# Performance work log

Measured on AMD Instinct MI355X. Metric: run time of the kernel, lower is better.

Reference implementation:

```python
import jax, jax.numpy as jnp
import numpy as np

N = 50000      # nodes
E = 800000     # directed edges (before self-loops)
IN = 128       # input feature dim
HID = 32       # per-head hidden channels
HEADS = 4
OUT = 16       # output classes
NEG_SLOPE = 0.2


def setup_inputs() -> dict:
    key = jax.random.key(0)
    ks = jax.random.split(key, 14)
    x = jax.random.normal(ks[0], (N, IN), jnp.float32)
    edge_index = jax.random.randint(ks[1], (2, E), 0, N, dtype=jnp.int64)

    def glorot(k, shape):
        fan = shape[0] + shape[-1]
        s = np.sqrt(6.0 / fan).astype(np.float32)
        return jax.random.uniform(k, shape, jnp.float32, -s, s)

    return {
        "x": x,
        "edge_index": edge_index,
        # layer 0: IN -> HEADS*HID
        "W1": glorot(ks[2], (IN, HEADS * HID)),
        "a_src1": glorot(ks[3], (HEADS, HID)),
        "a_dst1": glorot(ks[4], (HEADS, HID)),
        "b1": jnp.zeros((HEADS * HID,), jnp.float32),
        # layer 1: HEADS*HID -> HEADS*HID
        "W2": glorot(ks[5], (HEADS * HID, HEADS * HID)),
        "a_src2": glorot(ks[6], (HEADS, HID)),
        "a_dst2": glorot(ks[7], (HEADS, HID)),
        "b2": jnp.zeros((HEADS * HID,), jnp.float32),
        # layer 2: HEADS*HID -> OUT, heads=1
        "W3": glorot(ks[8], (HEADS * HID, OUT)),
        "a_src3": glorot(ks[9], (1, OUT)),
        "a_dst3": glorot(ks[10], (1, OUT)),
        "b3": jnp.zeros((OUT,), jnp.float32),
    }


def _gat_layer(x, src, dst, W, a_s, a_d, b):
    """One PyG-style GATConv (eval mode). src/dst include self-loops."""
    H, C = a_s.shape
    h = (x @ W).reshape(N, H, C)                       # [N,H,C]
    e_src = jnp.einsum('nhc,hc->nh', h, a_s)           # [N,H]
    e_dst = jnp.einsum('nhc,hc->nh', h, a_d)
    e = jax.nn.leaky_relu(e_src[src] + e_dst[dst], NEG_SLOPE)   # [E',H]
    # segment softmax over incoming edges of each target node
    m = jax.ops.segment_max(e, dst, num_segments=N)    # [N,H]
    p = jnp.exp(e - m[dst])
    denom = jax.ops.segment_sum(p, dst, num_segments=N)
    alpha = p / (denom[dst] + 1e-16)                   # [E',H]
    out = jax.ops.segment_sum(alpha[:, :, None] * h[src], dst, num_segments=N)
    return out.reshape(N, H * C) + b


def reference(x, edge_index, W1, a_src1, a_dst1, b1, W2, a_src2, a_dst2, b2,
              W3, a_src3, a_dst3, b3):
    loops = jnp.arange(N, dtype=edge_index.dtype)
    src = jnp.concatenate([edge_index[0], loops])
    dst = jnp.concatenate([edge_index[1], loops])
    h = jax.nn.relu(_gat_layer(x, src, dst, W1, a_src1, a_dst1, b1))
    h = jax.nn.relu(_gat_layer(h, src, dst, W2, a_src2, a_dst2, b2))
    return _gat_layer(h, src, dst, W3, a_src3, a_dst3, b3)   # [N, OUT]
```

## Files before the change

### kernel.cpp

```cpp
#include <hip/hip_runtime.h>

#define NODES 50000
#define EDGES 800000
#define EPLUS (EDGES + NODES)
#define GEMMBLK 782
#define FILLBLK 3321
#define CAP 64

__device__ __forceinline__ float ld_f(const void* p, int isbf, size_t i) {
    if (isbf) return __uint_as_float(((unsigned)((const unsigned short*)p)[i]) << 16);
    return ((const float*)p)[i];
}
__device__ __forceinline__ int ld_idx(const int* ei, int i64, int elem) {
    int v = i64 ? ei[(size_t)elem * 2] : ei[elem];
    v = v < 0 ? 0 : v;
    return v >= NODES ? NODES - 1 : v;
}
__device__ __forceinline__ unsigned short f2bf(float f) {
    unsigned u = __float_as_uint(f);
    u = u + 0x7FFFu + ((u >> 16) & 1u);
    return (unsigned short)(u >> 16);
}
__device__ __forceinline__ unsigned pack2bf(float a, float b) {
    return (unsigned)f2bf(a) | ((unsigned)f2bf(b) << 16);
}
__device__ __forceinline__ float bflo(unsigned u) { return __uint_as_float(u << 16); }
__device__ __forceinline__ float bfhi(unsigned u) { return __uint_as_float(u & 0xFFFF0000u); }

__device__ __forceinline__ void detect_flags(const unsigned* xw, const int* eiw,
                                             int* sh, int& isbf, int& i64) {
    const int t = threadIdx.x;
    if (t < 2) sh[t] = 0;
    __syncthreads();
    if (t < 256) {
        unsigned lo = xw[t] & 0xFFFFu;
        int e = (int)((lo >> 7) & 0xFF);
        if (lo == 0u || (e >= 90 && e <= 140)) atomicAdd(&sh[0], 1);
    }
    if (t < 64) {
        if (eiw[2 * t + 1] == 0) atomicAdd(&sh[1], 1);
    }
    __syncthreads();
    isbf = sh[0] > 200 ? 1 : 0;
    i64  = sh[1] > 48 ? 1 : 0;
}

#define O_W1 0
#define O_AS1 16384
#define O_AD1 16512
#define O_B1 16640
#define O_W2 16768
#define O_AS2 33152
#define O_AD2 33280
#define O_B2 33408
#define O_W3 33536
#define O_AS3 35584
#define O_AD3 35600
#define O_B3 35616
#define W_TOTAL 35632

__global__ __launch_bounds__(256, 4) void k_fillgemm1(
        const unsigned* __restrict__ xraw, const int* __restrict__ ei,
        const void* w1, const void* as1, const void* ad1, const void* b1,
        const void* w2, const void* as2, const void* ad2, const void* b2,
        const void* w3, const void* as3, const void* ad3, const void* b3,
        float* __restrict__ Wc,
        unsigned short* __restrict__ hout, float* __restrict__ es, float* __restrict__ ed,
        int* __restrict__ cnt, unsigned short* __restrict__ col) {
    __shared__ int sh[2];
    const int t = threadIdx.x;
    int isbf, i64;
    detect_flags(xraw, ei, sh, isbf, i64);

    if (blockIdx.x >= GEMMBLK) {
        const int f = (blockIdx.x - GEMMBLK) * 256 + t;
        if (f < W_TOTAL) {
            const int sz[12] = {16384,128,128,128,16384,128,128,128,2048,16,16,16};
            const void* ps[12] = {w1,as1,ad1,b1,w2,as2,ad2,b2,w3,as3,ad3,b3};
            int off = 0;
#pragma unroll
            for (int s = 0; s < 12; ++s) {
                if (f >= off && f < off + sz[s]) Wc[f] = ld_f(ps[s], isbf, f - off);
                off += sz[s];
            }
        }
        if (f >= EPLUS) return;
        int s, d;
        if (f < EDGES) {
            s = ld_idx(ei, i64, f);
            d = ld_idx(ei, i64, EDGES + f);
        } else s = d = f - EDGES;
        int slot = atomicAdd(&cnt[d], 1);
        if (slot < CAP) col[d * CAP + slot] = (unsigned short)s;
        return;
    }

    __shared__ float Xl[32][68];
    __shared__ float Wl[32][128];
    const int rowBase = blockIdx.x * 64;
    const int tx = t & 15, ty = t >> 4;
    const int cA = tx * 4, cB = 64 + tx * 4;

    float acc[4][8];
#pragma unroll
    for (int r = 0; r < 4; ++r)
#pragma unroll
        for (int j = 0; j < 8; ++j) acc[r][j] = 0.f;

    for (int k0 = 0; k0 < 128; k0 += 32) {
        __syncthreads();
        if (!isbf) {
            const float4* Wg = (const float4*)((const float*)w1 + k0 * 128);
            float4* Wl4 = (float4*)&Wl[0][0];
#pragma unroll
            for (int j = 0; j < 4; ++j) Wl4[t + 256 * j] = Wg[t + 256 * j];
#pragma unroll
            for (int j = 0; j < 2; ++j) {
                int f = t + 256 * j;
                int r = f >> 3;
                int kk = (f & 7) * 4;
                int gr = rowBase + r;
                if (gr >= NODES) gr = NODES - 1;
                float4 v = *(const float4*)((const float*)xraw + (size_t)gr * 128 + k0 + kk);
                Xl[kk][r] = v.x; Xl[kk+1][r] = v.y; Xl[kk+2][r] = v.z; Xl[kk+3][r] = v.w;
            }
        } else {
            float* Wf = &Wl[0][0];
#pragma unroll
            for (int j = 0; j < 4; ++j) {
                int f = t + 256 * j;
#pragma unroll
                for (int i = 0; i < 4; ++i)
                    Wf[f * 4 + i] = ld_f(w1, 1, (size_t)(k0 * 128) + f * 4 + i);
            }
#pragma unroll
            for (int j = 0; j < 2; ++j) {
                int f = t + 256 * j;
                int r = f >> 3;
                int kk = (f & 7) * 4;
                int gr = rowBase + r;
                if (gr >= NODES) gr = NODES - 1;
#pragma unroll
                for (int i = 0; i < 4; ++i)
                    Xl[kk + i][r] = ld_f(xraw, 1, (size_t)gr * 128 + k0 + kk + i);
            }
        }
        __syncthreads();
#pragma unroll 4
        for (int k = 0; k < 32; ++k) {
            const float4 xa = *(const float4*)&Xl[k][ty * 4];
            const float4 wa = *(const float4*)&Wl[k][cA];
            const float4 wb = *(const float4*)&Wl[k][cB];
            const float xs[4] = {xa.x, xa.y, xa.z, xa.w};
            const float ws[8] = {wa.x, wa.y, wa.z, wa.w, wb.x, wb.y, wb.z, wb.w};
#pragma unroll
            for (int r = 0; r < 4; ++r)
#pragma unroll
                for (int j = 0; j < 8; ++j)
                    acc[r][j] += xs[r] * ws[j];
        }
    }

    float asA[4], asB[4], adA[4], adB[4];
#pragma unroll
    for (int j = 0; j < 4; ++j) {
        asA[j] = ld_f(as1, isbf, cA + j); asB[j] = ld_f(as1, isbf, cB + j);
        adA[j] = ld_f(ad1, isbf, cA + j); adB[j] = ld_f(ad1, isbf, cB + j);
    }
    const int hA = tx >> 3;
#pragma unroll
    for (int r = 0; r < 4; ++r) {
        const int row = rowBase + ty * 4 + r;
        const bool ok = row < NODES;
        if (ok) {
            uint2 pA = {pack2bf(acc[r][0], acc[r][1]), pack2bf(acc[r][2], acc[r][3])};
            uint2 pB = {pack2bf(acc[r][4], acc[r][5]), pack2bf(acc[r][6], acc[r][7])};
            *(uint2*)&hout[(size_t)row * 128 + cA] = pA;
            *(uint2*)&hout[(size_t)row * 128 + cB] = pB;
        }
        float seA = acc[r][0]*asA[0] + acc[r][1]*asA[1] + acc[r][2]*asA[2] + acc[r][3]*asA[3];
        float seB = acc[r][4]*asB[0] + acc[r][5]*asB[1] + acc[r][6]*asB[2] + acc[r][7]*asB[3];
        float sdA = acc[r][0]*adA[0] + acc[r][1]*adA[1] + acc[r][2]*adA[2] + acc[r][3]*adA[3];
        float sdB = acc[r][4]*adB[0] + acc[r][5]*adB[1] + acc[r][6]*adB[2] + acc[r][7]*adB[3];
#pragma unroll
        for (int off = 1; off < 8; off <<= 1) {
            seA += __shfl_xor(seA, off);
            seB += __shfl_xor(seB, off);
            sdA += __shfl_xor(sdA, off);
            sdB += __shfl_xor(sdB, off);
        }
        if (ok && (tx & 7) == 0) {
            es[row * 4 + hA]     = seA;
            es[row * 4 + 2 + hA] = seB;
            ed[row * 4 + hA]     = sdA;
            ed[row * 4 + 2 + hA] = sdB;
        }
    }
}

__global__ __launch_bounds__(256, 4) void k_gemm128(
        const unsigned short* __restrict__ in, const float* __restrict__ W,
        const float* __restrict__ a_s, const float* __restrict__ a_d,
        unsigned short* __restrict__ hout, float* __restrict__ es, float* __restrict__ ed) {
    __shared__ float Xl[32][68];
    __shared__ float Wl[32][128];
    const int t = threadIdx.x;
    const int rowBase = blockIdx.x * 64;
    const int tx = t & 15, ty = t >> 4;
    const int cA = tx * 4, cB = 64 + tx * 4;

    float acc[4][8];
#pragma unroll
    for (int r = 0; r < 4; ++r)
#pragma unroll
        for (int j = 0; j < 8; ++j) acc[r][j] = 0.f;

    for (int k0 = 0; k0 < 128; k0 += 32) {
        __syncthreads();
        const float4* Wg = (const float4*)(W + k0 * 128);
        float4* Wl4 = (float4*)&Wl[0][0];
#pragma unroll
        for (int j = 0; j < 4; ++j) Wl4[t + 256 * j] = Wg[t + 256 * j];
#pragma unroll
        for (int j = 0; j < 2; ++j) {
            int f = t + 256 * j;
            int r = f >> 3;
            int kk = (f & 7) * 4;
            int gr = rowBase + r;
            if (gr >= NODES) gr = NODES - 1;
            uint2 v = *(const uint2*)(in + (size_t)gr * 128 + k0 + kk);
            Xl[kk][r] = bflo(v.x); Xl[kk+1][r] = bfhi(v.x);
            Xl[kk+2][r] = bflo(v.y); Xl[kk+3][r] = bfhi(v.y);
        }
        __syncthreads();
#pragma unroll 4
        for (int k = 0; k < 32; ++k) {
            const float4 xa = *(const float4*)&Xl[k][ty * 4];
            const float4 wa = *(const float4*)&Wl[k][cA];
            const float4 wb = *(const float4*)&Wl[k][cB];
            const float xs[4] = {xa.x, xa.y, xa.z, xa.w};
            const float ws[8] = {wa.x, wa.y, wa.z, wa.w, wb.x, wb.y, wb.z, wb.w};
#pragma unroll
            for (int r = 0; r < 4; ++r)
#pragma unroll
                for (int j = 0; j < 8; ++j)
                    acc[r][j] += xs[r] * ws[j];
        }
    }

    float asA[4], asB[4], adA[4], adB[4];
#pragma unroll
    for (int j = 0; j < 4; ++j) {
        asA[j] = a_s[cA + j]; asB[j] = a_s[cB + j];
        adA[j] = a_d[cA + j]; adB[j] = a_d[cB + j];
    }
    const int hA = tx >> 3;
#pragma unroll
    for (int r = 0; r < 4; ++r) {
        const int row = rowBase + ty * 4 + r;
        const bool ok = row < NODES;
        if (ok) {
            uint2 pA = {pack2bf(acc[r][0], acc[r][1]), pack2bf(acc[r][2], acc[r][3])};
            uint2 pB = {pack2bf(acc[r][4], acc[r][5]), pack2bf(acc[r][6], acc[r][7])};
            *(uint2*)&hout[(size_t)row * 128 + cA] = pA;
            *(uint2*)&hout[(size_t)row * 128 + cB] = pB;
        }
        float seA = acc[r][0]*asA[0] + acc[r][1]*asA[1] + acc[r][2]*asA[2] + acc[r][3]*asA[3];
        float seB = acc[r][4]*asB[0] + acc[r][5]*asB[1] + acc[r][6]*asB[2] + acc[r][7]*asB[3];
        float sdA = acc[r][0]*adA[0] + acc[r][1]*adA[1] + acc[r][2]*adA[2] + acc[r][3]*adA[3];
        float sdB = acc[r][4]*adB[0] + acc[r][5]*adB[1] + acc[r][6]*adB[2] + acc[r][7]*adB[3];
#pragma unroll
        for (int off = 1; off < 8; off <<= 1) {
            seA += __shfl_xor(seA, off);
            seB += __shfl_xor(seB, off);
            sdA += __shfl_xor(sdA, off);
            sdB += __shfl_xor(sdB, off);
        }
        if (ok && (tx & 7) == 0) {
            es[row * 4 + hA]     = seA;
            es[row * 4 + 2 + hA] = seB;
            ed[row * 4 + hA]     = sdA;
            ed[row * 4 + 2 + hA] = sdB;
        }
    }
}

__global__ __launch_bounds__(256, 2) void k_gemm16(
        const unsigned short* __restrict__ in, const float* __restrict__ W,
        const float* __restrict__ a_s, const float* __restrict__ a_d,
        unsigned short* __restrict__ hout, float* __restrict__ es, float* __restrict__ ed) {
    __shared__ float Xl[32][132];
    __shared__ float Wl[128 * 16];
    const int t = threadIdx.x;
    const int rowBase = blockIdx.x * 128;
    const int tx = t & 3, ty = t >> 2;

    ((float4*)Wl)[t] = ((const float4*)W)[t];
    ((float4*)Wl)[t + 256] = ((const float4*)W)[t + 256];

    float acc[2][4];
#pragma unroll
    for (int r = 0; r < 2; ++r)
#pragma unroll
        for (int j = 0; j < 4; ++j) acc[r][j] = 0.f;

    for (int k0 = 0; k0 < 128; k0 += 32) {
        __syncthreads();
#pragma unroll
        for (int j = 0; j < 4; ++j) {
            int f = t + 256 * j;
            int r = f >> 3;
            int kk = (f & 7) * 4;
            int gr = rowBase + r;
            if (gr >= NODES) gr = NODES - 1;
            uint2 v = *(const uint2*)(in + (size_t)gr * 128 + k0 + kk);
            Xl[kk][r] = bflo(v.x); Xl[kk+1][r] = bfhi(v.x);
            Xl[kk+2][r] = bflo(v.y); Xl[kk+3][r] = bfhi(v.y);
        }
        __syncthreads();
#pragma unroll 4
        for (int k = 0; k < 32; ++k) {
            const float2 xv = *(const float2*)&Xl[k][ty * 2];
            const float4 wv = *(const float4*)&Wl[(k0 + k) * 16 + tx * 4];
            acc[0][0] += xv.x * wv.x; acc[0][1] += xv.x * wv.y;
            acc[0][2] += xv.x * wv.z; acc[0][3] += xv.x * wv.w;
            acc[1][0] += xv.y * wv.x; acc[1][1] += xv.y * wv.y;
            acc[1][2] += xv.y * wv.z; acc[1][3] += xv.y * wv.w;
        }
    }

    const float4 asv = *(const float4*)&a_s[tx * 4];
    const float4 adv = *(const float4*)&a_d[tx * 4];
#pragma unroll
    for (int r = 0; r < 2; ++r) {
        const int row = rowBase + ty * 2 + r;
        const bool ok = row < NODES;
        if (ok) {
            uint2 pk = {pack2bf(acc[r][0], acc[r][1]), pack2bf(acc[r][2], acc[r][3])};
            *(uint2*)&hout[(size_t)row * 16 + tx * 4] = pk;
        }
        float se = acc[r][0]*asv.x + acc[r][1]*asv.y + acc[r][2]*asv.z + acc[r][3]*asv.w;
        float sd = acc[r][0]*adv.x + acc[r][1]*adv.y + acc[r][2]*adv.z + acc[r][3]*adv.w;
#pragma unroll
        for (int off = 1; off < 4; off <<= 1) {
            se += __shfl_xor(se, off);
            sd += __shfl_xor(sd, off);
        }
        if (ok && tx == 0) { es[row] = se; ed[row] = sd; }
    }
}

__global__ void k_gather4(const int* __restrict__ cnt, const unsigned short* __restrict__ col,
                          const float* __restrict__ es, const float* __restrict__ ed,
                          const unsigned short* __restrict__ hfeat,
                          const float* __restrict__ bias, unsigned short* __restrict__ outb) {
    const int nd = blockIdx.x * 4 + (threadIdx.x >> 6);
    if (nd >= NODES) return;
    const int lane = threadIdx.x & 63;
    int deg = cnt[nd]; deg = deg < CAP ? deg : CAP;
    const int start = nd * CAP;

    const int esub = lane >> 4;
    const int c = lane & 15;
    const int myh = c >> 2;
    const float edh = ed[nd * 4 + myh];
    const uint4* __restrict__ h4 = (const uint4*)hfeat;
    float a[8] = {0.f,0.f,0.f,0.f,0.f,0.f,0.f,0.f};
    float den = 0.f;

    int e = esub;
    for (; e + 4 < deg; e += 8) {
        int s0 = col[start + e];
        int s1 = col[start + e + 4];
        uint4 u0 = h4[(size_t)s0 * 16 + c];
        uint4 u1 = h4[(size_t)s1 * 16 + c];
        float v0 = es[s0 * 4 + myh] + edh; v0 = v0 > 0.f ? v0 : 0.2f * v0;
        float v1 = es[s1 * 4 + myh] + edh; v1 = v1 > 0.f ? v1 : 0.2f * v1;
        float p0 = __expf(v0);
        float p1 = __expf(v1);
        den += p0 + p1;
        a[0] += p0 * bflo(u0.x) + p1 * bflo(u1.x);
        a[1] += p0 * bfhi(u0.x) + p1 * bfhi(u1.x);
        a[2] += p0 * bflo(u0.y) + p1 * bflo(u1.y);
        a[3] += p0 * bfhi(u0.y) + p1 * bfhi(u1.y);
        a[4] += p0 * bflo(u0.z) + p1 * bflo(u1.z);
        a[5] += p0 * bfhi(u0.z) + p1 * bfhi(u1.z);
        a[6] += p0 * bflo(u0.w) + p1 * bflo(u1.w);
        a[7] += p0 * bfhi(u0.w) + p1 * bfhi(u1.w);
    }
    for (; e < deg; e += 4) {
        int s0 = col[start + e];
        uint4 u0 = h4[(size_t)s0 * 16 + c];
        float v0 = es[s0 * 4 + myh] + edh; v0 = v0 > 0.f ? v0 : 0.2f * v0;
        float p0 = __expf(v0);
        den += p0;
        a[0] += p0 * bflo(u0.x);
        a[1] += p0 * bfhi(u0.x);
        a[2] += p0 * bflo(u0.y);
        a[3] += p0 * bfhi(u0.y);
        a[4] += p0 * bflo(u0.z);
        a[5] += p0 * bfhi(u0.z);
        a[6] += p0 * bflo(u0.w);
        a[7] += p0 * bfhi(u0.w);
    }
    den += __shfl_xor(den, 16);
    den += __shfl_xor(den, 32);
#pragma unroll
    for (int j = 0; j < 8; ++j) {
        a[j] += __shfl_xor(a[j], 16);
        a[j] += __shfl_xor(a[j], 32);
    }

    if (esub == 0) {
        const float inv = 1.f / (den + 1e-16f);
        float4 b0 = ((const float4*)bias)[c * 2];
        float4 b1 = ((const float4*)bias)[c * 2 + 1];
        float o0 = a[0]*inv + b0.x, o1 = a[1]*inv + b0.y;
        float o2 = a[2]*inv + b0.z, o3 = a[3]*inv + b0.w;
        float o4 = a[4]*inv + b1.x, o5 = a[5]*inv + b1.y;
        float o6 = a[6]*inv + b1.z, o7 = a[7]*inv + b1.w;
        o0 = o0 > 0.f ? o0 : 0.f;  o1 = o1 > 0.f ? o1 : 0.f;
        o2 = o2 > 0.f ? o2 : 0.f;  o3 = o3 > 0.f ? o3 : 0.f;
        o4 = o4 > 0.f ? o4 : 0.f;  o5 = o5 > 0.f ? o5 : 0.f;
        o6 = o6 > 0.f ? o6 : 0.f;  o7 = o7 > 0.f ? o7 : 0.f;
        uint4 pk = {pack2bf(o0, o1), pack2bf(o2, o3), pack2bf(o4, o5), pack2bf(o6, o7)};
        ((uint4*)outb)[(size_t)nd * 16 + c] = pk;
    }
}

__global__ void k_gather1(const int* __restrict__ cnt, const unsigned short* __restrict__ col,
                          const float* __restrict__ es, const float* __restrict__ ed,
                          const unsigned short* __restrict__ hfeat,
                          const float* __restrict__ bias, float* __restrict__ outf) {
    const int nd = blockIdx.x * 4 + (threadIdx.x >> 6);
    if (nd >= NODES) return;
    const int lane = threadIdx.x & 63;
    int deg = cnt[nd]; deg = deg < CAP ? deg : CAP;
    const int start = nd * CAP;

    const float edv = ed[nd];
    const int esub = lane >> 3;
    const int c = lane & 7;
    const unsigned* __restrict__ h1 = (const unsigned*)hfeat;
    float a0 = 0.f, a1 = 0.f, den = 0.f;

    int e = esub;
    for (; e + 8 < deg; e += 16) {
        int s0 = col[start + e];
        int s1 = col[start + e + 8];
        unsigned u0 = h1[(size_t)s0 * 8 + c];
        unsigned u1 = h1[(size_t)s1 * 8 + c];
        float v0 = es[s0] + edv; v0 = v0 > 0.f ? v0 : 0.2f * v0;
        float v1 = es[s1] + edv; v1 = v1 > 0.f ? v1 : 0.2f * v1;
        float p0 = __expf(v0);
        float p1 = __expf(v1);
        den += p0 + p1;
        a0 += p0 * bflo(u0) + p1 * bflo(u1);
        a1 += p0 * bfhi(u0) + p1 * bfhi(u1);
    }
    for (; e < deg; e += 8) {
        int s0 = col[start + e];
        unsigned u0 = h1[(size_t)s0 * 8 + c];
        float v0 = es[s0] + edv; v0 = v0 > 0.f ? v0 : 0.2f * v0;
        float p0 = __expf(v0);
        den += p0;
        a0 += p0 * bflo(u0);
        a1 += p0 * bfhi(u0);
    }
    den += __shfl_xor(den, 8);  a0 += __shfl_xor(a0, 8);  a1 += __shfl_xor(a1, 8);
    den += __shfl_xor(den, 16); a0 += __shfl_xor(a0, 16); a1 += __shfl_xor(a1, 16);
    den += __shfl_xor(den, 32); a0 += __shfl_xor(a0, 32); a1 += __shfl_xor(a1, 32);
    if (lane < 8) {
        const float inv = 1.f / (den + 1e-16f);
        float2 b = ((const float2*)bias)[c];
        ((float2*)outf)[(size_t)nd * 8 + c] = make_float2(a0 * inv + b.x, a1 * inv + b.y);
    }
}

static inline int gs(long n) { return (int)((n + 255) / 256); }

extern "C" void kernel_launch(void* const* d_in, const int* in_sizes, int n_in,
                              void* d_out, int out_size, void* d_ws, size_t ws_size,
                              hipStream_t stream) {
    const int* ei = (const int*)d_in[1];
    const unsigned* xraw = (const unsigned*)d_in[0];
    float* out = (float*)d_out;

    char* p = (char*)d_ws;
    unsigned short* Xb  = (unsigned short*)p; p += (size_t)NODES * 128 * 2;
    unsigned short* A   = (unsigned short*)p; p += (size_t)NODES * 128 * 2;
    float*          es  = (float*)p;          p += (size_t)NODES * 4 * 4;
    float*          ed  = (float*)p;          p += (size_t)NODES * 4 * 4;
    float*          Wc  = (float*)p;          p += (size_t)W_TOTAL * 4;
    int*            cnt = (int*)p;            p += (size_t)NODES * 4;
    unsigned short* col = (unsigned short*)p; p += (size_t)NODES * CAP * 2;

    hipMemsetAsync(cnt, 0, (size_t)NODES * 4, stream);

    k_fillgemm1<<<GEMMBLK + FILLBLK, 256, 0, stream>>>(
        xraw, ei,
        d_in[2], d_in[3], d_in[4], d_in[5],
        d_in[6], d_in[7], d_in[8], d_in[9],
        d_in[10], d_in[11], d_in[12], d_in[13],
        Wc, A, es, ed, cnt, col);

    const int ggrid = (NODES + 3) / 4;
    k_gather4<<<ggrid, 256, 0, stream>>>(cnt, col, es, ed, A, Wc + O_B1, Xb);
    k_gemm128<<<(NODES + 63) / 64, 256, 0, stream>>>(Xb, Wc + O_W2, Wc + O_AS2, Wc + O_AD2,
                                                     A, es, ed);
    k_gather4<<<ggrid, 256, 0, stream>>>(cnt, col, es, ed, A, Wc + O_B2, Xb);
    k_gemm16<<<(NODES + 127) / 128, 256, 0, stream>>>(Xb, Wc + O_W3, Wc + O_AS3, Wc + O_AD3,
                                                      A, es, ed);
    k_gather1<<<ggrid, 256, 0, stream>>>(cnt, col, es, ed, A, Wc + O_B3, out);
}
```

Before: 286.4 us.

## Move the three dense GEMMs onto bf16 MFMA with split hi/lo weights

The scalar FP32 tiled GEMMs for all three layers become MFMA 16x16x32 bf16 kernels. A new prep kernel converts the weights into fragment-ordered hi/lo bf16 pairs, and for fp32 inputs the first layer's activations are split the same way, so an error-compensated three-product scheme keeps accuracy close to fp32. The prep kernel also takes over zeroing the edge counters and the weight copy, which removes the separate memset. This adds an extra launch and extra MFMA work for the compensation terms, and activation stores become scalar 16-bit writes instead of packed ones.

```diff
diff --git a/kernel.cpp b/kernel.cpp
--- a/kernel.cpp
+++ b/kernel.cpp
@@ -6,6 +6,10 @@
 #define GEMMBLK 782
 #define FILLBLK 3321
 #define CAP 64
+
+typedef __attribute__((ext_vector_type(8))) short bf16x8;
+typedef __attribute__((ext_vector_type(4))) float f32x4;
+typedef __attribute__((ext_vector_type(4))) short short4v;
 
 __device__ __forceinline__ float ld_f(const void* p, int isbf, size_t i) {
     if (isbf) return __uint_as_float(((unsigned)((const unsigned short*)p)[i]) << 16);
@@ -59,12 +63,71 @@
 #define O_B3 35616
 #define W_TOTAL 35632
 
-__global__ __launch_bounds__(256, 4) void k_fillgemm1(
+#define PB_CNT 196
+#define PB_WC 140
+#define PB_F1 64
+#define PB_F2 64
+#define PB_F3 8
+#define PREP_GRID (PB_CNT + PB_WC + PB_F1 + PB_F2 + PB_F3)
+
+__global__ __launch_bounds__(256) void k_prep(
         const unsigned* __restrict__ xraw, const int* __restrict__ ei,
         const void* w1, const void* as1, const void* ad1, const void* b1,
         const void* w2, const void* as2, const void* ad2, const void* b2,
         const void* w3, const void* as3, const void* ad3, const void* b3,
-        float* __restrict__ Wc,
+        float* __restrict__ Wc, int* __restrict__ cnt,
+        unsigned short* __restrict__ W1fh, unsigned short* __restrict__ W1fl,
+        unsigned short* __restrict__ W2fh, unsigned short* __restrict__ W2fl,
+        unsigned short* __restrict__ W3fh, unsigned short* __restrict__ W3fl) {
+    __shared__ int sh[2];
+    const int t = threadIdx.x;
+    int isbf, i64;
+    detect_flags(xraw, ei, sh, isbf, i64);
+    (void)i64;
+
+    int b = blockIdx.x;
+    if (b < PB_CNT) {
+        int i = b * 256 + t;
+        if (i < NODES) cnt[i] = 0;
+        return;
+    }
+    b -= PB_CNT;
+    if (b < PB_WC) {
+        const int f = b * 256 + t;
+        if (f < W_TOTAL) {
+            const int sz[12] = {16384,128,128,128,16384,128,128,128,2048,16,16,16};
+            const void* ps[12] = {w1,as1,ad1,b1,w2,as2,ad2,b2,w3,as3,ad3,b3};
+            int off = 0;
+#pragma unroll
+            for (int s = 0; s < 12; ++s) {
+                if (f >= off && f < off + sz[s]) Wc[f] = ld_f(ps[s], isbf, f - off);
+                off += sz[s];
+            }
+        }
+        return;
+    }
+    b -= PB_WC;
+    const void* wsrc; unsigned short *fh, *fl; int ncols; int e;
+    if (b < PB_F1)                { wsrc = w1; fh = W1fh; fl = W1fl; ncols = 128; e = b * 256 + t; }
+    else if (b < PB_F1 + PB_F2)   { wsrc = w2; fh = W2fh; fl = W2fl; ncols = 128; e = (b - PB_F1) * 256 + t; }
+    else                          { wsrc = w3; fh = W3fh; fl = W3fl; ncols = 16;  e = (b - PB_F1 - PB_F2) * 256 + t; }
+    const int j = e & 7, l = (e >> 3) & 63;
+    int nf, kc;
+    if (ncols == 128) { nf = (e >> 9) & 7; kc = e >> 12; }
+    else              { nf = 0;            kc = (e >> 9) & 3; }
+    const int k = kc * 32 + (l >> 4) * 4 + (j & 3) + (j >> 2) * 16;
+    const int n = nf * 16 + (l & 15);
+    const float v = ld_f(wsrc, isbf, (size_t)k * ncols + n);
+    const unsigned short hi = f2bf(v);
+    const float res = v - __uint_as_float(((unsigned)hi) << 16);
+    fh[e] = hi;
+    fl[e] = f2bf(res);
+}
+
+__global__ __launch_bounds__(256, 4) void k_fillgemm1(
+        const unsigned* __restrict__ xraw, const int* __restrict__ ei,
+        const unsigned short* __restrict__ W1fh, const unsigned short* __restrict__ W1fl,
+        const float* __restrict__ Wc,
         unsigned short* __restrict__ hout, float* __restrict__ es, float* __restrict__ ed,
         int* __restrict__ cnt, unsigned short* __restrict__ col) {
     __shared__ int sh[2];
@@ -74,16 +137,6 @@
 
     if (blockIdx.x >= GEMMBLK) {
         const int f = (blockIdx.x - GEMMBLK) * 256 + t;
-        if (f < W_TOTAL) {
-            const int sz[12] = {16384,128,128,128,16384,128,128,128,2048,16,16,16};
-            const void* ps[12] = {w1,as1,ad1,b1,w2,as2,ad2,b2,w3,as3,ad3,b3};
-            int off = 0;
-#pragma unroll
-            for (int s = 0; s < 12; ++s) {
-                if (f >= off && f < off + sz[s]) Wc[f] = ld_f(ps[s], isbf, f - off);
-                off += sz[s];
-            }
-        }
         if (f >= EPLUS) return;
         int s, d;
         if (f < EDGES) {
@@ -95,258 +148,213 @@
         return;
     }
 
-    __shared__ float Xl[32][68];
-    __shared__ float Wl[32][128];
+    __shared__ unsigned short Ah[4 * 64 * 8];
+    __shared__ unsigned short Al[4 * 64 * 8];
     const int rowBase = blockIdx.x * 64;
-    const int tx = t & 15, ty = t >> 4;
-    const int cA = tx * 4, cB = 64 + tx * 4;
-
-    float acc[4][8];
-#pragma unroll
-    for (int r = 0; r < 4; ++r)
-#pragma unroll
-        for (int j = 0; j < 8; ++j) acc[r][j] = 0.f;
-
-    for (int k0 = 0; k0 < 128; k0 += 32) {
+    const int w = t >> 6, lane = t & 63;
+
+    f32x4 acc[4][2];
+#pragma unroll
+    for (int mf = 0; mf < 4; ++mf)
+#pragma unroll
+        for (int nn = 0; nn < 2; ++nn) acc[mf][nn] = (f32x4){0.f, 0.f, 0.f, 0.f};
+
+    for (int kc = 0; kc < 4; ++kc) {
         __syncthreads();
-        if (!isbf) {
-            const float4* Wg = (const float4*)((const float*)w1 + k0 * 128);
-            float4* Wl4 = (float4*)&Wl[0][0];
-#pragma unroll
-            for (int j = 0; j < 4; ++j) Wl4[t + 256 * j] = Wg[t + 256 * j];
-#pragma unroll
-            for (int j = 0; j < 2; ++j) {
-                int f = t + 256 * j;
-                int r = f >> 3;
-                int kk = (f & 7) * 4;
-                int gr = rowBase + r;
-                if (gr >= NODES) gr = NODES - 1;
-                float4 v = *(const float4*)((const float*)xraw + (size_t)gr * 128 + k0 + kk);
-                Xl[kk][r] = v.x; Xl[kk+1][r] = v.y; Xl[kk+2][r] = v.z; Xl[kk+3][r] = v.w;
-            }
-        } else {
-            float* Wf = &Wl[0][0];
-#pragma unroll
-            for (int j = 0; j < 4; ++j) {
-                int f = t + 256 * j;
-#pragma unroll
-                for (int i = 0; i < 4; ++i)
-                    Wf[f * 4 + i] = ld_f(w1, 1, (size_t)(k0 * 128) + f * 4 + i);
-            }
-#pragma unroll
-            for (int j = 0; j < 2; ++j) {
-                int f = t + 256 * j;
-                int r = f >> 3;
-                int kk = (f & 7) * 4;
-                int gr = rowBase + r;
-                if (gr >= NODES) gr = NODES - 1;
-#pragma unroll
-                for (int i = 0; i < 4; ++i)
-                    Xl[kk + i][r] = ld_f(xraw, 1, (size_t)gr * 128 + k0 + kk + i);
+#pragma unroll
+        for (int u = 0; u < 2; ++u) {
+            const int f = t + 256 * u;
+            const int r = f >> 3, c4 = f & 7;
+            int gr = rowBase + r; if (gr >= NODES) gr = NODES - 1;
+            const int mf = r >> 4;
+            const int l  = (r & 15) + 16 * (c4 & 3);
+            const int j0 = 4 * (c4 >> 2);
+            const int di = (mf * 64 + l) * 8 + j0;
+            if (!isbf) {
+                float4 v = *(const float4*)((const float*)xraw + (size_t)gr * 128 + kc * 32 + c4 * 4);
+                const unsigned short h0 = f2bf(v.x), h1 = f2bf(v.y), h2 = f2bf(v.z), h3 = f2bf(v.w);
+                short4v hv = {(short)h0, (short)h1, (short)h2, (short)h3};
+                *(short4v*)&Ah[di] = hv;
+                short4v lv = {(short)f2bf(v.x - __uint_as_float((unsigned)h0 << 16)),
+                              (short)f2bf(v.y - __uint_as_float((unsigned)h1 << 16)),
+                              (short)f2bf(v.z - __uint_as_float((unsigned)h2 << 16)),
+                              (short)f2bf(v.w - __uint_as_float((unsigned)h3 << 16))};
+                *(short4v*)&Al[di] = lv;
+            } else {
+                short4v v = *(const short4v*)((const unsigned short*)xraw + (size_t)gr * 128 + kc * 32 + c4 * 4);
+                *(short4v*)&Ah[di] = v;
             }
         }
         __syncthreads();
-#pragma unroll 4
-        for (int k = 0; k < 32; ++k) {
-            const float4 xa = *(const float4*)&Xl[k][ty * 4];
-            const float4 wa = *(const float4*)&Wl[k][cA];
-            const float4 wb = *(const float4*)&Wl[k][cB];
-            const float xs[4] = {xa.x, xa.y, xa.z, xa.w};
-            const float ws[8] = {wa.x, wa.y, wa.z, wa.w, wb.x, wb.y, wb.z, wb.w};
-#pragma unroll
-            for (int r = 0; r < 4; ++r)
-#pragma unroll
-                for (int j = 0; j < 8; ++j)
-                    acc[r][j] += xs[r] * ws[j];
-        }
-    }
-
-    float asA[4], asB[4], adA[4], adB[4];
-#pragma unroll
-    for (int j = 0; j < 4; ++j) {
-        asA[j] = ld_f(as1, isbf, cA + j); asB[j] = ld_f(as1, isbf, cB + j);
-        adA[j] = ld_f(ad1, isbf, cA + j); adB[j] = ld_f(ad1, isbf, cB + j);
-    }
-    const int hA = tx >> 3;
-#pragma unroll
-    for (int r = 0; r < 4; ++r) {
-        const int row = rowBase + ty * 4 + r;
-        const bool ok = row < NODES;
-        if (ok) {
-            uint2 pA = {pack2bf(acc[r][0], acc[r][1]), pack2bf(acc[r][2], acc[r][3])};
-            uint2 pB = {pack2bf(acc[r][4], acc[r][5]), pack2bf(acc[r][6], acc[r][7])};
-            *(uint2*)&hout[(size_t)row * 128 + cA] = pA;
-            *(uint2*)&hout[(size_t)row * 128 + cB] = pB;
-        }
-        float seA = acc[r][0]*asA[0] + acc[r][1]*asA[1] + acc[r][2]*asA[2] + acc[r][3]*asA[3];
-        float seB = acc[r][4]*asB[0] + acc[r][5]*asB[1] + acc[r][6]*asB[2] + acc[r][7]*asB[3];
-        float sdA = acc[r][0]*adA[0] + acc[r][1]*adA[1] + acc[r][2]*adA[2] + acc[r][3]*adA[3];
-        float sdB = acc[r][4]*adB[0] + acc[r][5]*adB[1] + acc[r][6]*adB[2] + acc[r][7]*adB[3];
-#pragma unroll
-        for (int off = 1; off < 8; off <<= 1) {
-            seA += __shfl_xor(seA, off);
-            seB += __shfl_xor(seB, off);
-            sdA += __shfl_xor(sdA, off);
-            sdB += __shfl_xor(sdB, off);
-        }
-        if (ok && (tx & 7) == 0) {
-            es[row * 4 + hA]     = seA;
-            es[row * 4 + 2 + hA] = seB;
-            ed[row * 4 + hA]     = sdA;
-            ed[row * 4 + 2 + hA] = sdB;
+        const int nA = 2 * w, nB = 2 * w + 1;
+        const bf16x8 bh0 = *(const bf16x8*)(W1fh + (((size_t)kc * 8 + nA) * 64 + lane) * 8);
+        const bf16x8 bh1 = *(const bf16x8*)(W1fh + (((size_t)kc * 8 + nB) * 64 + lane) * 8);
+        const bf16x8 bl0 = *(const bf16x8*)(W1fl + (((size_t)kc * 8 + nA) * 64 + lane) * 8);
+        const bf16x8 bl1 = *(const bf16x8*)(W1fl + (((size_t)kc * 8 + nB) * 64 + lane) * 8);
+#pragma unroll
+        for (int mf = 0; mf < 4; ++mf) {
+            const bf16x8 ah = *(const bf16x8*)&Ah[(mf * 64 + lane) * 8];
+            acc[mf][0] = __builtin_amdgcn_mfma_f32_16x16x32_bf16(ah, bh0, acc[mf][0], 0, 0, 0);
+            acc[mf][1] = __builtin_amdgcn_mfma_f32_16x16x32_bf16(ah, bh1, acc[mf][1], 0, 0, 0);
+            if (!isbf) {
+                const bf16x8 al = *(const bf16x8*)&Al[(mf * 64 + lane) * 8];
+                acc[mf][0] = __builtin_amdgcn_mfma_f32_16x16x32_bf16(ah, bl0, acc[mf][0], 0, 0, 0);
+                acc[mf][1] = __builtin_amdgcn_mfma_f32_16x16x32_bf16(ah, bl1, acc[mf][1], 0, 0, 0);
+                acc[mf][0] = __builtin_amdgcn_mfma_f32_16x16x32_bf16(al, bh0, acc[mf][0], 0, 0, 0);
+                acc[mf][1] = __builtin_amdgcn_mfma_f32_16x16x32_bf16(al, bh1, acc[mf][1], 0, 0, 0);
+            }
+        }
+    }
+
+    const int colA = 32 * w + (lane & 15), colB = colA + 16;
+    const float asA = Wc[O_AS1 + colA], asB = Wc[O_AS1 + colB];
+    const float adA = Wc[O_AD1 + colA], adB = Wc[O_AD1 + colB];
+    const int g = lane >> 4;
+#pragma unroll
+    for (int mf = 0; mf < 4; ++mf) {
+#pragma unroll
+        for (int r = 0; r < 4; ++r) {
+            const int row = rowBase + mf * 16 + 4 * g + r;
+            const bool ok = row < NODES;
+            const float vA = acc[mf][0][r], vB = acc[mf][1][r];
+            if (ok) {
+                hout[(size_t)row * 128 + colA] = f2bf(vA);
+                hout[(size_t)row * 128 + colB] = f2bf(vB);
+            }
+            float se = vA * asA + vB * asB;
+            float sd = vA * adA + vB * adB;
+#pragma unroll
+            for (int off = 1; off < 16; off <<= 1) {
+                se += __shfl_xor(se, off);
+                sd += __shfl_xor(sd, off);
+            }
+            if (ok && (lane & 15) == 0) {
+                es[row * 4 + w] = se;
+                ed[row * 4 + w] = sd;
+            }
         }
     }
 }
 
 __global__ __launch_bounds__(256, 4) void k_gemm128(
-        const unsigned short* __restrict__ in, const float* __restrict__ W,
+        const unsigned short* __restrict__ in,
+        const unsigned short* __restrict__ Wfh, const unsigned short* __restrict__ Wfl,
         const float* __restrict__ a_s, const float* __restrict__ a_d,
         unsigned short* __restrict__ hout, float* __restrict__ es, float* __restrict__ ed) {
-    __shared__ float Xl[32][68];
-    __shared__ float Wl[32][128];
+    __shared__ unsigned short Ah[4 * 64 * 8];
     const int t = threadIdx.x;
     const int rowBase = blockIdx.x * 64;
-    const int tx = t & 15, ty = t >> 4;
-    const int cA = tx * 4, cB = 64 + tx * 4;
-
-    float acc[4][8];
-#pragma unroll
-    for (int r = 0; r < 4; ++r)
-#pragma unroll
-        for (int j = 0; j < 8; ++j) acc[r][j] = 0.f;
-
-    for (int k0 = 0; k0 < 128; k0 += 32) {
+    const int w = t >> 6, lane = t & 63;
+
+    f32x4 acc[4][2];
+#pragma unroll
+    for (int mf = 0; mf < 4; ++mf)
+#pragma unroll
+        for (int nn = 0; nn < 2; ++nn) acc[mf][nn] = (f32x4){0.f, 0.f, 0.f, 0.f};
+
+    for (int kc = 0; kc < 4; ++kc) {
         __syncthreads();
-        const float4* Wg = (const float4*)(W + k0 * 128);
-        float4* Wl4 = (float4*)&Wl[0][0];
-#pragma unroll
-        for (int j = 0; j < 4; ++j) Wl4[t + 256 * j] = Wg[t + 256 * j];
-#pragma unroll
-        for (int j = 0; j < 2; ++j) {
-            int f = t + 256 * j;
-            int r = f >> 3;
-            int kk = (f & 7) * 4;
-            int gr = rowBase + r;
-            if (gr >= NODES) gr = NODES - 1;
-            uint2 v = *(const uint2*)(in + (size_t)gr * 128 + k0 + kk);
-            Xl[kk][r] = bflo(v.x); Xl[kk+1][r] = bfhi(v.x);
-            Xl[kk+2][r] = bflo(v.y); Xl[kk+3][r] = bfhi(v.y);
+#pragma unroll
+        for (int u = 0; u < 2; ++u) {
+            const int f = t + 256 * u;
+            const int r = f >> 3, c4 = f & 7;
+            int gr = rowBase + r; if (gr >= NODES) gr = NODES - 1;
+            const int di = ((r >> 4) * 64 + (r & 15) + 16 * (c4 & 3)) * 8 + 4 * (c4 >> 2);
+            short4v v = *(const short4v*)(in + (size_t)gr * 128 + kc * 32 + c4 * 4);
+            *(short4v*)&Ah[di] = v;
         }
         __syncthreads();
-#pragma unroll 4
-        for (int k = 0; k < 32; ++k) {
-            const float4 xa = *(const float4*)&Xl[k][ty * 4];
-            const float4 wa = *(const float4*)&Wl[k][cA];
-            const float4 wb = *(const float4*)&Wl[k][cB];
-            const float xs[4] = {xa.x, xa.y, xa.z, xa.w};
-            const float ws[8] = {wa.x, wa.y, wa.z, wa.w, wb.x, wb.y, wb.z, wb.w};
-#pragma unroll
-            for (int r = 0; r < 4; ++r)
-#pragma unroll
-                for (int j = 0; j < 8; ++j)
-                    acc[r][j] += xs[r] * ws[j];
-        }
-    }
-
-    float asA[4], asB[4], adA[4], adB[4];
-#pragma unroll
-    for (int j = 0; j < 4; ++j) {
-        asA[j] = a_s[cA + j]; asB[j] = a_s[cB + j];
-        adA[j] = a_d[cA + j]; adB[j] = a_d[cB + j];
-    }
-    const int hA = tx >> 3;
-#pragma unroll
-    for (int r = 0; r < 4; ++r) {
-        const int row = rowBase + ty * 4 + r;
-        const bool ok = row < NODES;
-        if (ok) {
-            uint2 pA = {pack2bf(acc[r][0], acc[r][1]), pack2bf(acc[r][2], acc[r][3])};
-            uint2 pB = {pack2bf(acc[r][4], acc[r][5]), pack2bf(acc[r][6], acc[r][7])};
-            *(uint2*)&hout[(size_t)row * 128 + cA] = pA;
-            *(uint2*)&hout[(size_t)row * 128 + cB] = pB;
-        }
-        float seA = acc[r][0]*asA[0] + acc[r][1]*asA[1] + acc[r][2]*asA[2] + acc[r][3]*asA[3];
-        float seB = acc[r][4]*asB[0] + acc[r][5]*asB[1] + acc[r][6]*asB[2] + acc[r][7]*asB[3];
-        float sdA = acc[r][0]*adA[0] + acc[r][1]*adA[1] + acc[r][2]*adA[2] + acc[r][3]*adA[3];
-        float sdB = acc[r][4]*adB[0] + acc[r][5]*adB[1] + acc[r][6]*adB[2] + acc[r][7]*adB[3];
-#pragma unroll
-        for (int off = 1; off < 8; off <<= 1) {
-            seA += __shfl_xor(seA, off);
-            seB += __shfl_xor(seB, off);
-            sdA += __shfl_xor(sdA, off);
-            sdB += __shfl_xor(sdB, off);
-        }
-        if (ok && (tx & 7) == 0) {
-            es[row * 4 + hA]     = seA;
-            es[row * 4 + 2 + hA] = seB;
-            ed[row * 4 + hA]     = sdA;
-            ed[row * 4 + 2 + hA] = sdB;
-        }
-    }
-}
-
-__global__ __launch_bounds__(256, 2) void k_gemm16(
-        const unsigned short* __restrict__ in, const float* __restrict__ W,
+        const int nA = 2 * w, nB = 2 * w + 1;
+        const bf16x8 bh0 = *(const bf16x8*)(Wfh + (((size_t)kc * 8 + nA) * 64 + lane) * 8);
+        const bf16x8 bh1 = *(const bf16x8*)(Wfh + (((size_t)kc * 8 + nB) * 64 + lane) * 8);
+        const bf16x8 bl0 = *(const bf16x8*)(Wfl + (((size_t)kc * 8 + nA) * 64 + lane) * 8);
+        const bf16x8 bl1 = *(const bf16x8*)(Wfl + (((size_t)kc * 8 + nB) * 64 + lane) * 8);
+#pragma unroll
+        for (int mf = 0; mf < 4; ++mf) {
+            const bf16x8 ah = *(const bf16x8*)&Ah[(mf * 64 + lane) * 8];
+            acc[mf][0] = __builtin_amdgcn_mfma_f32_16x16x32_bf16(ah, bh0, acc[mf][0], 0, 0, 0);
+            acc[mf][1] = __builtin_amdgcn_mfma_f32_16x16x32_bf16(ah, bh1, acc[mf][1], 0, 0, 0);
+            acc[mf][0] = __builtin_amdgcn_mfma_f32_16x16x32_bf16(ah, bl0, acc[mf][0], 0, 0, 0);
+            acc[mf][1] = __builtin_amdgcn_mfma_f32_16x16x32_bf16(ah, bl1, acc[mf][1], 0, 0, 0);
+        }
+    }
+
+    const int colA = 32 * w + (lane & 15), colB = colA + 16;
+    const float asA = a_s[colA], asB = a_s[colB];
+    const float adA = a_d[colA], adB = a_d[colB];
+    const int g = lane >> 4;
+#pragma unroll
+    for (int mf = 0; mf < 4; ++mf) {
+#pragma unroll
+        for (int r = 0; r < 4; ++r) {
+            const int row = rowBase + mf * 16 + 4 * g + r;
+            const bool ok = row < NODES;
+            const float vA = acc[mf][0][r], vB = acc[mf][1][r];
+            if (ok) {
+                hout[(size_t)row * 128 + colA] = f2bf(vA);
+                hout[(size_t)row * 128 + colB] = f2bf(vB);
+            }
+            float se = vA * asA + vB * asB;
+            float sd = vA * adA + vB * adB;
+#pragma unroll
+            for (int off = 1; off < 16; off <<= 1) {
+                se += __shfl_xor(se, off);
+                sd += __shfl_xor(sd, off);
+            }
+            if (ok && (lane & 15) == 0) {
+                es[row * 4 + w] = se;
+                ed[row * 4 + w] = sd;
+            }
+        }
+    }
+}
+
+__global__ __launch_bounds__(256, 4) void k_gemm16(
+        const unsigned short* __restrict__ in,
+        const unsigned short* __restrict__ Wfh, const unsigned short* __restrict__ Wfl,
         const float* __restrict__ a_s, const float* __restrict__ a_d,
         unsigned short* __restrict__ hout, float* __restrict__ es, float* __restrict__ ed) {
-    __shared__ float Xl[32][132];
-    __shared__ float Wl[128 * 16];
+    __shared__ unsigned short Ah[4 * 64 * 8];
     const int t = threadIdx.x;
-    const int rowBase = blockIdx.x * 128;
-    const int tx = t & 3, ty = t >> 2;
-
-    ((float4*)Wl)[t] = ((const float4*)W)[t];
-    ((float4*)Wl)[t + 256] = ((const float4*)W)[t + 256];
-
-    float acc[2][4];
-#pragma unroll
-    for (int r = 0; r < 2; ++r)
-#pragma unroll
-        for (int j = 0; j < 4; ++j) acc[r][j] = 0.f;
-
-    for (int k0 = 0; k0 < 128; k0 += 32) {
+    const int rowBase = blockIdx.x * 64;
+    const int w = t >> 6, lane = t & 63;
+
+    f32x4 acc = (f32x4){0.f, 0.f, 0.f, 0.f};
+
+    for (int kc = 0; kc < 4; ++kc) {
         __syncthreads();
 #pragma unroll
-        for (int j = 0; j < 4; ++j) {
-            int f = t + 256 * j;
-            int r = f >> 3;
-            int kk = (f & 7) * 4;
-            int gr = rowBase + r;
-            if (gr >= NODES) gr = NODES - 1;
-            uint2 v = *(const uint2*)(in + (size_t)gr * 128 + k0 + kk);
-            Xl[kk][r] = bflo(v.x); Xl[kk+1][r] = bfhi(v.x);
-            Xl[kk+2][r] = bflo(v.y); Xl[kk+3][r] = bfhi(v.y);
+        for (int u = 0; u < 2; ++u) {
+            const int f = t + 256 * u;
+            const int r = f >> 3, c4 = f & 7;
+            int gr = rowBase + r; if (gr >= NODES) gr = NODES - 1;
+            const int di = ((r >> 4) * 64 + (r & 15) + 16 * (c4 & 3)) * 8 + 4 * (c4 >> 2);
+            short4v v = *(const short4v*)(in + (size_t)gr * 128 + kc * 32 + c4 * 4);
+            *(short4v*)&Ah[di] = v;
         }
         __syncthreads();
-#pragma unroll 4
-        for (int k = 0; k < 32; ++k) {
-            const float2 xv = *(const float2*)&Xl[k][ty * 2];
-            const float4 wv = *(const float4*)&Wl[(k0 + k) * 16 + tx * 4];
-            acc[0][0] += xv.x * wv.x; acc[0][1] += xv.x * wv.y;
-            acc[0][2] += xv.x * wv.z; acc[0][3] += xv.x * wv.w;
-            acc[1][0] += xv.y * wv.x; acc[1][1] += xv.y * wv.y;
-            acc[1][2] += xv.y * wv.z; acc[1][3] += xv.y * wv.w;
-        }
-    }
-
-    const float4 asv = *(const float4*)&a_s[tx * 4];
-    const float4 adv = *(const float4*)&a_d[tx * 4];
-#pragma unroll
-    for (int r = 0; r < 2; ++r) {
-        const int row = rowBase + ty * 2 + r;
+        const bf16x8 bh = *(const bf16x8*)(Wfh + ((size_t)kc * 64 + lane) * 8);
+        const bf16x8 bl = *(const bf16x8*)(Wfl + ((size_t)kc * 64 + lane) * 8);
+        const bf16x8 ah = *(const bf16x8*)&Ah[(w * 64 + lane) * 8];
+        acc = __builtin_amdgcn_mfma_f32_16x16x32_bf16(ah, bh, acc, 0, 0, 0);
+        acc = __builtin_amdgcn_mfma_f32_16x16x32_bf16(ah, bl, acc, 0, 0, 0);
+    }
+
+    const int c = lane & 15, g = lane >> 4;
+    const float asv = a_s[c], adv = a_d[c];
+#pragma unroll
+    for (int r = 0; r < 4; ++r) {
+        const int row = rowBase + w * 16 + 4 * g + r;
         const bool ok = row < NODES;
-        if (ok) {
-            uint2 pk = {pack2bf(acc[r][0], acc[r][1]), pack2bf(acc[r][2], acc[r][3])};
-            *(uint2*)&hout[(size_t)row * 16 + tx * 4] = pk;
-        }
-        float se = acc[r][0]*asv.x + acc[r][1]*asv.y + acc[r][2]*asv.z + acc[r][3]*asv.w;
-        float sd = acc[r][0]*adv.x + acc[r][1]*adv.y + acc[r][2]*adv.z + acc[r][3]*adv.w;
-#pragma unroll
-        for (int off = 1; off < 4; off <<= 1) {
+        if (ok) hout[(size_t)row * 16 + c] = f2bf(acc[r]);
+        float se = acc[r] * asv;
+        float sd = acc[r] * adv;
+#pragma unroll
+        for (int off = 1; off < 16; off <<= 1) {
             se += __shfl_xor(se, off);
             sd += __shfl_xor(sd, off);
         }
-        if (ok && tx == 0) { es[row] = se; ed[row] = sd; }
+        if (ok && c == 0) { es[row] = se; ed[row] = sd; }
     }
 }
 
@@ -477,8 +485,6 @@
     }
 }
 
-static inline int gs(long n) { return (int)((n + 255) / 256); }
-
 extern "C" void kernel_launch(void* const* d_in, const int* in_sizes, int n_in,
                               void* d_out, int out_size, void* d_ws, size_t ws_size,
                               hipStream_t stream) {
@@ -494,22 +500,27 @@
     float*          Wc  = (float*)p;          p += (size_t)W_TOTAL * 4;
     int*            cnt = (int*)p;            p += (size_t)NODES * 4;
     unsigned short* col = (unsigned short*)p; p += (size_t)NODES * CAP * 2;
-
-    hipMemsetAsync(cnt, 0, (size_t)NODES * 4, stream);
-
-    k_fillgemm1<<<GEMMBLK + FILLBLK, 256, 0, stream>>>(
+    unsigned short* W1fh = (unsigned short*)p; p += 16384 * 2;
+    unsigned short* W1fl = (unsigned short*)p; p += 16384 * 2;
+    unsigned short* W2fh = (unsigned short*)p; p += 16384 * 2;
+    unsigned short* W2fl = (unsigned short*)p; p += 16384 * 2;
+    unsigned short* W3fh = (unsigned short*)p; p += 2048 * 2;
+    unsigned short* W3fl = (unsigned short*)p; p += 2048 * 2;
+
+    k_prep<<<PREP_GRID, 256, 0, stream>>>(
         xraw, ei,
         d_in[2], d_in[3], d_in[4], d_in[5],
         d_in[6], d_in[7], d_in[8], d_in[9],
         d_in[10], d_in[11], d_in[12], d_in[13],
-        Wc, A, es, ed, cnt, col);
+        Wc, cnt, W1fh, W1fl, W2fh, W2fl, W3fh, W3fl);
+
+    k_fillgemm1<<<GEMMBLK + FILLBLK, 256, 0, stream>>>(
+        xraw, ei, W1fh, W1fl, Wc, A, es, ed, cnt, col);
 
     const int ggrid = (NODES + 3) / 4;
     k_gather4<<<ggrid, 256, 0, stream>>>(cnt, col, es, ed, A, Wc + O_B1, Xb);
-    k_gemm128<<<(NODES + 63) / 64, 256, 0, stream>>>(Xb, Wc + O_W2, Wc + O_AS2, Wc + O_AD2,
-                                                     A, es, ed);
+    k_gemm128<<<GEMMBLK, 256, 0, stream>>>(Xb, W2fh, W2fl, Wc + O_AS2, Wc + O_AD2, A, es, ed);
     k_gather4<<<ggrid, 256, 0, stream>>>(cnt, col, es, ed, A, Wc + O_B2, Xb);
-    k_gemm16<<<(NODES + 127) / 128, 256, 0, stream>>>(Xb, Wc + O_W3, Wc + O_AS3, Wc + O_AD3,
-                                                      A, es, ed);
+    k_gemm16<<<GEMMBLK, 256, 0, stream>>>(Xb, W3fh, W3fl, Wc + O_AS3, Wc + O_AD3, A, es, ed);
     k_gather1<<<ggrid, 256, 0, stream>>>(cnt, col, es, ed, A, Wc + O_B3, out);
 }
```

Result: faster. 257.5 us (-10.1%).
